# Kernel tuning notes

Measured on AMD Instinct MI355X. Metric: run time of the kernel, lower is better.

The kernel has to match this reference:

```python
import jax, jax.numpy as jnp
import numpy as np


def apply_rope(x):
    # x: [B, T, H, D]
    T, D = x.shape[1], x.shape[3]
    inv_freq = 1.0 / (10000.0 ** (jnp.arange(0, D, 2, dtype=jnp.float32) / D))  # [D/2]
    t = jnp.arange(T, dtype=jnp.float32)
    freqs = jnp.outer(t, inv_freq)  # [T, D/2]
    sin_f = jnp.sin(freqs)[None, :, None, :]
    cos_f = jnp.cos(freqs)[None, :, None, :]
    x1, x2 = jnp.split(x, 2, axis=-1)
    return jnp.concatenate([x1 * cos_f - x2 * sin_f, x1 * sin_f + x2 * cos_f], axis=-1)


def setup_inputs() -> dict:
    key = jax.random.key(0)
    ks = jax.random.split(key, 5)
    B, T, D = 8, 8192, 128
    s = 1.0 / np.sqrt(D)
    return {
        "x": jax.random.normal(ks[0], (B, T, D), dtype=jnp.float32),
        "Wq": jax.random.normal(ks[1], (D, D), dtype=jnp.float32) * s,
        "bq": jnp.zeros((D,), dtype=jnp.float32),
        "Wk": jax.random.normal(ks[2], (D, D), dtype=jnp.float32) * s,
        "bk": jnp.zeros((D,), dtype=jnp.float32),
        "Wv": jax.random.normal(ks[3], (D, D), dtype=jnp.float32) * s,
        "bv": jnp.zeros((D,), dtype=jnp.float32),
        "Wo": jax.random.normal(ks[4], (D, D), dtype=jnp.float32) * s,
        "bo": jnp.zeros((D,), dtype=jnp.float32),
    }


def reference(x, Wq, bq, Wk, bk, Wv, bv, Wo, bo):
    n_heads = 8
    B, T, d_model = x.shape
    head_dim = d_model // n_heads

    q = (x @ Wq + bq).reshape(B, T, n_heads, head_dim)
    k = (x @ Wk + bk).reshape(B, T, n_heads, head_dim)
    v = (x @ Wv + bv).reshape(B, T, n_heads, head_dim)

    q = jax.nn.elu(apply_rope(q)) + 1.0
    k = jax.nn.elu(apply_rope(k)) + 1.0

    # non-causal linear attention: context = sum_t k_t v_t^T per head
    context = jnp.einsum("bthd,bthe->bhde", k, v)            # [B,H,Dh,Dh]
    out = jnp.einsum("bthd,bhde->bthe", q, context)           # [B,T,H,Dh]
    k_sum = jnp.sum(k, axis=1)                                  # [B,H,Dh]
    z = 1.0 / (jnp.einsum("bthd,bhd->bth", q, k_sum) + 1e-6)  # [B,T,H]
    out = out * z[..., None]

    out = out.reshape(B, T, d_model)
    return out @ Wo + bo
```

## Files before the change

kernel.cpp:

```cpp
#include <hip/hip_runtime.h>
#include <hip/hip_bf16.h>


typedef __attribute__((ext_vector_type(8))) short short8;
typedef __attribute__((ext_vector_type(4))) float floatx4;

#define DEV __device__ __forceinline__
#define MFMA __builtin_amdgcn_mfma_f32_16x16x32_bf16

DEV unsigned short bfh(float f) {
  unsigned int x = __float_as_uint(f);
  x += 0x7fffu + ((x >> 16) & 1u);
  return (unsigned short)(x >> 16);
}
DEV float bfdec(unsigned short u) { return __uint_as_float(((unsigned int)u) << 16); }
DEV void splitf(float f, unsigned short& h, unsigned short& l) {
  h = bfh(f);
  l = bfh(f - bfdec(h));
}
DEV void split8(const float* p, short8& h8, short8& l8) {
  float4 a = *(const float4*)p;
  float4 b = *(const float4*)(p + 4);
  float v[8] = {a.x, a.y, a.z, a.w, b.x, b.y, b.z, b.w};
  union { short8 s; unsigned short u[8]; } H, L;
#pragma unroll
  for (int i = 0; i < 8; ++i) splitf(v[i], H.u[i], L.u[i]);
  h8 = H.s; l8 = L.s;
}

DEV void xpose_frag(floatx4 m0, floatx4 m1, int lane16, int quad,
                    short8& hi, short8& lo) {
  union { short8 s; unsigned short u[8]; } H, L;
#pragma unroll
  for (int j = 0; j < 8; ++j) {
    int srcLane = lane16 + (((quad & 1) * 2 + (j >> 2)) << 4);
    float vA = __shfl(m0[j & 3], srcLane, 64);
    float vB = __shfl(m1[j & 3], srcLane, 64);
    float v = (quad < 2) ? vA : vB;
    splitf(v, H.u[j], L.u[j]);
  }
  hi = H.s; lo = L.s;
}

DEV void async16(const void* g, void* l) {
  __builtin_amdgcn_global_load_lds(
      (const __attribute__((address_space(1))) unsigned int*)g,
      (__attribute__((address_space(3))) unsigned int*)l, 16, 0, 0);
}

__global__ void k_prep(const float* __restrict__ Wq, const float* __restrict__ Wk,
                       const float* __restrict__ Wv,
                       unsigned short* __restrict__ WTh, unsigned short* __restrict__ WTl,
                       float* __restrict__ ctxz) {
  int gid = blockIdx.x * 256 + threadIdx.x;
  if (gid < 6144) {
    int mat = gid >> 11, r = gid & 2047, n = r >> 4, k0 = (r & 15) * 8;
    const float* W = (mat == 0) ? Wq : (mat == 1) ? Wk : Wv;
    union { uint4 q; unsigned short u[8]; } oh, ol;
#pragma unroll
    for (int i = 0; i < 8; ++i) splitf(W[(size_t)(k0 + i) * 128 + n], oh.u[i], ol.u[i]);
    *(uint4*)&WTh[mat * 16384 + n * 128 + k0] = oh.q;
    *(uint4*)&WTl[mat * 16384 + n * 128 + k0] = ol.q;
  } else if (gid < 6144 + 17408) {
    ctxz[gid - 6144] = 0.0f;
  }
}

__global__ __launch_bounds__(512) void k_qkv(
    const float* __restrict__ x,
    const unsigned short* __restrict__ WTh, const unsigned short* __restrict__ WTl,
    const float* __restrict__ bq, const float* __restrict__ bk, const float* __restrict__ bv,
    float* __restrict__ ctx, float* __restrict__ ksum,
    unsigned short* __restrict__ qws) {
  __shared__ unsigned short xh[64 * 136], xl[64 * 136];
  __shared__ float rc[64][9], rs[64][9];
  const int tid = threadIdx.x;
  const int row0 = blockIdx.x * 64;
  const int b = row0 >> 13;
  const int t0 = row0 & 8191;

  {
    int r = tid >> 3, j = tid & 7;
    float invf = 1.0f / powf(10000.0f, (float)j * 0.125f);
    float s, c;
    sincosf((float)(t0 + r) * invf, &s, &c);
    rc[r][j] = c; rs[r][j] = s;
  }
  {
    int r = tid >> 3, cg = (tid & 7) * 16;
    const float* xp = x + (size_t)(row0 + r) * 128 + cg;
    short8 h0, l0, h1, l1;
    split8(xp, h0, l0);
    split8(xp + 8, h1, l1);
    *(short8*)&xh[r * 136 + cg] = h0;
    *(short8*)&xh[r * 136 + cg + 8] = h1;
    *(short8*)&xl[r * 136 + cg] = l0;
    *(short8*)&xl[r * 136 + cg + 8] = l1;
  }
  __syncthreads();

  const int l = tid & 63, w = tid >> 6;
  const int lane16 = l & 15, quad = l >> 4;

  floatx4 acc[3][4];
#pragma unroll
  for (int i = 0; i < 3; ++i)
#pragma unroll
    for (int j = 0; j < 4; ++j) acc[i][j] = (floatx4){0.f, 0.f, 0.f, 0.f};

  size_t wbase[3];
#pragma unroll
  for (int mat = 0; mat < 3; ++mat)
    wbase[mat] = (size_t)mat * 16384 + (size_t)(w * 16 + lane16) * 128 + quad * 8;

  short8 wh[2][3], wl[2][3];
#pragma unroll
  for (int mat = 0; mat < 3; ++mat) {
    wh[0][mat] = *(const short8*)(WTh + wbase[mat]);
    wl[0][mat] = *(const short8*)(WTl + wbase[mat]);
  }

#pragma unroll
  for (int ks = 0; ks < 4; ++ks) {
    const int cur = ks & 1, nxt = cur ^ 1;
    if (ks < 3) {
#pragma unroll
      for (int mat = 0; mat < 3; ++mat) {
        wh[nxt][mat] = *(const short8*)(WTh + wbase[mat] + (ks + 1) * 32);
        wl[nxt][mat] = *(const short8*)(WTl + wbase[mat] + (ks + 1) * 32);
      }
    }
    short8 afh[4], afl[4];
#pragma unroll
    for (int mt = 0; mt < 4; ++mt) {
      int off = (mt * 16 + lane16) * 136 + ks * 32 + quad * 8;
      afh[mt] = *(const short8*)&xh[off];
      afl[mt] = *(const short8*)&xl[off];
    }
#pragma unroll
    for (int mat = 0; mat < 3; ++mat) {
#pragma unroll
      for (int mt = 0; mt < 4; ++mt) {
        acc[mat][mt] = MFMA(afh[mt], wh[cur][mat], acc[mat][mt], 0, 0, 0);
        acc[mat][mt] = MFMA(afl[mt], wh[cur][mat], acc[mat][mt], 0, 0, 0);
        acc[mat][mt] = MFMA(afh[mt], wl[cur][mat], acc[mat][mt], 0, 0, 0);
      }
    }
  }

  {
    int col = w * 16 + lane16;
    float bias[3] = {bq[col], bk[col], bv[col]};
#pragma unroll
    for (int mat = 0; mat < 3; ++mat)
#pragma unroll
      for (int mt = 0; mt < 4; ++mt)
#pragma unroll
        for (int r = 0; r < 4; ++r) acc[mat][mt][r] += bias[mat];
  }

  {
    const int d = lane16, j = d & 7;
#pragma unroll
    for (int mt = 0; mt < 4; ++mt) {
      float cc[4], ss[4];
#pragma unroll
      for (int r = 0; r < 4; ++r) {
        int tl = mt * 16 + quad * 4 + r;
        cc[r] = rc[tl][j]; ss[r] = rs[tl][j];
      }
#pragma unroll
      for (int mat = 0; mat < 2; ++mat) {
#pragma unroll
        for (int r = 0; r < 4; ++r) {
          float v = acc[mat][mt][r];
          float p = __shfl_xor(v, 8);
          float nv = (d < 8) ? (v * cc[r] - p * ss[r]) : (p * ss[r] + v * cc[r]);
          acc[mat][mt][r] = (nv > 0.f) ? (nv + 1.f) : __expf(nv);
        }
      }
    }
  }

  {
    float s = 0.f;
#pragma unroll
    for (int mt = 0; mt < 4; ++mt)
#pragma unroll
      for (int r = 0; r < 4; ++r) s += acc[1][mt][r];
    s += __shfl_xor(s, 16);
    s += __shfl_xor(s, 32);
    if (l < 16) atomicAdd(&ksum[(b * 8 + w) * 16 + lane16], s);
  }

#pragma unroll
  for (int mt = 0; mt < 4; ++mt)
#pragma unroll
    for (int r = 0; r < 4; ++r)
      qws[(size_t)(row0 + mt * 16 + quad * 4 + r) * 128 + w * 16 + lane16] =
          bfh(acc[0][mt][r]);

  {
    floatx4 c = (floatx4){0.f, 0.f, 0.f, 0.f};
#pragma unroll
    for (int ks2 = 0; ks2 < 2; ++ks2) {
      short8 kh, kl, vh, vl;
      xpose_frag(acc[1][ks2 * 2], acc[1][ks2 * 2 + 1], lane16, quad, kh, kl);
      xpose_frag(acc[2][ks2 * 2], acc[2][ks2 * 2 + 1], lane16, quad, vh, vl);
      c = MFMA(kh, vh, c, 0, 0, 0);
      c = MFMA(kl, vh, c, 0, 0, 0);
      c = MFMA(kh, vl, c, 0, 0, 0);
    }
#pragma unroll
    for (int r = 0; r < 4; ++r)
      atomicAdd(&ctx[((size_t)(b * 8 + w) * 16 + quad * 4 + r) * 16 + lane16], c[r]);
  }
}

__global__ void k_mprep(const float* __restrict__ Wo, const float* __restrict__ ctx,
                        unsigned short* __restrict__ MTh, unsigned short* __restrict__ MTl) {
  int gid = blockIdx.x * 256 + threadIdx.x;
  int b = gid >> 11, r = gid & 2047, oc = r >> 4, qcg = r & 15;
  int h = qcg >> 1, d0 = (qcg & 1) * 8;
  const float* C = ctx + (size_t)(b * 8 + h) * 256;
  float m[8] = {0.f, 0.f, 0.f, 0.f, 0.f, 0.f, 0.f, 0.f};
#pragma unroll 4
  for (int e = 0; e < 16; ++e) {
    float wv = Wo[(size_t)(h * 16 + e) * 128 + oc];
#pragma unroll
    for (int i = 0; i < 8; ++i) m[i] += C[(d0 + i) * 16 + e] * wv;
  }
  union { uint4 q; unsigned short u[8]; } oh, ol;
#pragma unroll
  for (int i = 0; i < 8; ++i) splitf(m[i], oh.u[i], ol.u[i]);
  int grp = (((oc >> 4) * 4 + (qcg >> 2)) * 64) + (qcg & 3) * 16 + (oc & 15);
  *(uint4*)&MTh[(size_t)b * 16384 + grp * 8] = oh.q;
  *(uint4*)&MTl[(size_t)b * 16384 + grp * 8] = ol.q;
}

__global__ __launch_bounds__(256) void k_zout(
    const unsigned short* __restrict__ qws,
    const unsigned short* __restrict__ MTh, const unsigned short* __restrict__ MTl,
    const float* __restrict__ bo, const float* __restrict__ ksum,
    float* __restrict__ out) {
  __shared__ __align__(16) unsigned short mh[16384], ml[16384];
  __shared__ float ksumS[128], boS[128];
  const int tid = threadIdx.x;
  const int row0 = blockIdx.x * 128;
  const int b = row0 >> 13;
  const int l = tid & 63, w = tid >> 6;
  const int lane16 = l & 15, quad = l >> 4;

  {
    const char* gh = (const char*)(MTh + (size_t)b * 16384);
    const char* gl = (const char*)(MTl + (size_t)b * 16384);
#pragma unroll
    for (int i = 0; i < 8; ++i) {
      int off = (i * 4 + w) * 1024 + l * 16;
      async16(gh + off, (char*)mh + off);
      async16(gl + off, (char*)ml + off);
    }
  }
  if (tid < 128) ksumS[tid] = ksum[b * 128 + tid];
  else boS[tid - 128] = bo[tid - 128];
  __syncthreads();

  short8 ah[2][4], al[2][4];
#pragma unroll
  for (int mt2 = 0; mt2 < 2; ++mt2) {
    int trow = row0 + w * 32 + mt2 * 16 + lane16;
#pragma unroll
    for (int ks = 0; ks < 4; ++ks) {
      union { short8 s8; unsigned short u[8]; } qq;
      qq.s8 = *(const short8*)&qws[(size_t)trow * 128 + ks * 32 + quad * 8];
      int kb = ks * 32 + quad * 8;
      float s = 0.f;
#pragma unroll
      for (int j = 0; j < 8; ++j) s += bfdec(qq.u[j]) * ksumS[kb + j];
      s += __shfl_xor(s, 16);
      float z = 1.0f / (s + 1e-6f);
      union { short8 s8; unsigned short u[8]; } H, L;
#pragma unroll
      for (int j = 0; j < 8; ++j) splitf(bfdec(qq.u[j]) * z, H.u[j], L.u[j]);
      ah[mt2][ks] = H.s8;
      al[mt2][ks] = L.s8;
    }
  }

  floatx4 oacc[2][8];
#pragma unroll
  for (int i = 0; i < 2; ++i)
#pragma unroll
    for (int j = 0; j < 8; ++j) oacc[i][j] = (floatx4){0.f, 0.f, 0.f, 0.f};

#pragma unroll
  for (int nt = 0; nt < 8; ++nt) {
#pragma unroll
    for (int ks = 0; ks < 4; ++ks) {
      int moff = ((nt * 4 + ks) * 64 + l) * 8;
      short8 wbh = *(const short8*)&mh[moff];
      short8 wbl = *(const short8*)&ml[moff];
#pragma unroll
      for (int mt2 = 0; mt2 < 2; ++mt2) {
        oacc[mt2][nt] = MFMA(ah[mt2][ks], wbh, oacc[mt2][nt], 0, 0, 0);
        oacc[mt2][nt] = MFMA(al[mt2][ks], wbh, oacc[mt2][nt], 0, 0, 0);
        oacc[mt2][nt] = MFMA(ah[mt2][ks], wbl, oacc[mt2][nt], 0, 0, 0);
      }
    }
  }

#pragma unroll
  for (int nt = 0; nt < 8; ++nt) {
    int oc = nt * 16 + lane16;
    float bb = boS[oc];
#pragma unroll
    for (int mt2 = 0; mt2 < 2; ++mt2)
#pragma unroll
      for (int r = 0; r < 4; ++r) {
        int t = row0 + w * 32 + mt2 * 16 + quad * 4 + r;
        out[(size_t)t * 128 + oc] = oacc[mt2][nt][r] + bb;
      }
  }
}

extern "C" void kernel_launch(void* const* d_in, const int* in_sizes, int n_in,
                              void* d_out, int out_size, void* d_ws, size_t ws_size,
                              hipStream_t stream) {
  const float* x  = (const float*)d_in[0];
  const float* Wq = (const float*)d_in[1];
  const float* bq = (const float*)d_in[2];
  const float* Wk = (const float*)d_in[3];
  const float* bk = (const float*)d_in[4];
  const float* Wv = (const float*)d_in[5];
  const float* bv = (const float*)d_in[6];
  const float* Wo = (const float*)d_in[7];
  const float* bo = (const float*)d_in[8];
  float* out = (float*)d_out;

  unsigned short* qws = (unsigned short*)d_ws;
  unsigned short* WTh = qws + 8388608;
  unsigned short* WTl = WTh + 49152;
  float* ctx  = (float*)(WTl + 49152);
  float* ksum = ctx + 16384;
  unsigned short* MTh = (unsigned short*)(ksum + 1024);
  unsigned short* MTl = MTh + 131072;

  k_prep<<<92, 256, 0, stream>>>(Wq, Wk, Wv, WTh, WTl, ctx);
  k_qkv<<<1024, 512, 0, stream>>>(x, WTh, WTl, bq, bk, bv, ctx, ksum, qws);
  k_mprep<<<64, 256, 0, stream>>>(Wo, ctx, MTh, MTl);
  k_zout<<<512, 256, 0, stream>>>(qws, MTh, MTl, bo, ksum, out);
}
```

Measured before the change: 159.4 us.

## Drop x low-part split in QKV, precompute RoPE table, widen zout blocks

The QKV projection now rounds x to a single bf16 part instead of a hi/lo split. This removes one of the three MFMAs per tile, the xl shared buffer and the split arithmetic, at the cost of accuracy on the activation side. RoPE sin/cos values are precomputed once into a workspace table in k_prep rather than evaluated per block with powf/sincosf. k_zout moves to 512 threads with one 16-row tile per wave, lowering register use per thread in exchange for more waves per block.

```diff
diff --git a/kernel.cpp b/kernel.cpp
--- a/kernel.cpp
+++ b/kernel.cpp
@@ -17,15 +17,6 @@
 DEV void splitf(float f, unsigned short& h, unsigned short& l) {
   h = bfh(f);
   l = bfh(f - bfdec(h));
-}
-DEV void split8(const float* p, short8& h8, short8& l8) {
-  float4 a = *(const float4*)p;
-  float4 b = *(const float4*)(p + 4);
-  float v[8] = {a.x, a.y, a.z, a.w, b.x, b.y, b.z, b.w};
-  union { short8 s; unsigned short u[8]; } H, L;
-#pragma unroll
-  for (int i = 0; i < 8; ++i) splitf(v[i], H.u[i], L.u[i]);
-  h8 = H.s; l8 = L.s;
 }
 
 DEV void xpose_frag(floatx4 m0, floatx4 m1, int lane16, int quad,
@@ -51,7 +42,7 @@
 __global__ void k_prep(const float* __restrict__ Wq, const float* __restrict__ Wk,
                        const float* __restrict__ Wv,
                        unsigned short* __restrict__ WTh, unsigned short* __restrict__ WTl,
-                       float* __restrict__ ctxz) {
+                       float* __restrict__ ctxz, float2* __restrict__ ropeT) {
   int gid = blockIdx.x * 256 + threadIdx.x;
   if (gid < 6144) {
     int mat = gid >> 11, r = gid & 2047, n = r >> 4, k0 = (r & 15) * 8;
@@ -63,16 +54,23 @@
     *(uint4*)&WTl[mat * 16384 + n * 128 + k0] = ol.q;
   } else if (gid < 6144 + 17408) {
     ctxz[gid - 6144] = 0.0f;
+  } else if (gid < 6144 + 17408 + 65536) {
+    int r = gid - 23552;
+    int t = r >> 3, j = r & 7;
+    float invf = 1.0f / powf(10000.0f, (float)j * 0.125f);
+    float s, c;
+    sincosf((float)t * invf, &s, &c);
+    ropeT[r] = make_float2(c, s);
   }
 }
 
 __global__ __launch_bounds__(512) void k_qkv(
-    const float* __restrict__ x,
+    const float* __restrict__ x, const float2* __restrict__ ropeT,
     const unsigned short* __restrict__ WTh, const unsigned short* __restrict__ WTl,
     const float* __restrict__ bq, const float* __restrict__ bk, const float* __restrict__ bv,
     float* __restrict__ ctx, float* __restrict__ ksum,
     unsigned short* __restrict__ qws) {
-  __shared__ unsigned short xh[64 * 136], xl[64 * 136];
+  __shared__ unsigned short xh[64 * 136];
   __shared__ float rc[64][9], rs[64][9];
   const int tid = threadIdx.x;
   const int row0 = blockIdx.x * 64;
@@ -81,21 +79,23 @@
 
   {
     int r = tid >> 3, j = tid & 7;
-    float invf = 1.0f / powf(10000.0f, (float)j * 0.125f);
-    float s, c;
-    sincosf((float)(t0 + r) * invf, &s, &c);
-    rc[r][j] = c; rs[r][j] = s;
+    float2 cs = ropeT[(t0 + r) * 8 + j];
+    rc[r][j] = cs.x; rs[r][j] = cs.y;
   }
   {
     int r = tid >> 3, cg = (tid & 7) * 16;
     const float* xp = x + (size_t)(row0 + r) * 128 + cg;
-    short8 h0, l0, h1, l1;
-    split8(xp, h0, l0);
-    split8(xp + 8, h1, l1);
-    *(short8*)&xh[r * 136 + cg] = h0;
-    *(short8*)&xh[r * 136 + cg + 8] = h1;
-    *(short8*)&xl[r * 136 + cg] = l0;
-    *(short8*)&xl[r * 136 + cg + 8] = l1;
+    float4 a = *(const float4*)xp;
+    float4 b4 = *(const float4*)(xp + 4);
+    float4 c4 = *(const float4*)(xp + 8);
+    float4 d4 = *(const float4*)(xp + 12);
+    float v[16] = {a.x, a.y, a.z, a.w, b4.x, b4.y, b4.z, b4.w,
+                   c4.x, c4.y, c4.z, c4.w, d4.x, d4.y, d4.z, d4.w};
+    union { short8 s; unsigned short u[8]; } h0, h1;
+#pragma unroll
+    for (int i = 0; i < 8; ++i) { h0.u[i] = bfh(v[i]); h1.u[i] = bfh(v[8 + i]); }
+    *(short8*)&xh[r * 136 + cg] = h0.s;
+    *(short8*)&xh[r * 136 + cg + 8] = h1.s;
   }
   __syncthreads();
 
@@ -130,19 +130,15 @@
         wl[nxt][mat] = *(const short8*)(WTl + wbase[mat] + (ks + 1) * 32);
       }
     }
-    short8 afh[4], afl[4];
-#pragma unroll
-    for (int mt = 0; mt < 4; ++mt) {
-      int off = (mt * 16 + lane16) * 136 + ks * 32 + quad * 8;
-      afh[mt] = *(const short8*)&xh[off];
-      afl[mt] = *(const short8*)&xl[off];
-    }
+    short8 afh[4];
+#pragma unroll
+    for (int mt = 0; mt < 4; ++mt)
+      afh[mt] = *(const short8*)&xh[(mt * 16 + lane16) * 136 + ks * 32 + quad * 8];
 #pragma unroll
     for (int mat = 0; mat < 3; ++mat) {
 #pragma unroll
       for (int mt = 0; mt < 4; ++mt) {
         acc[mat][mt] = MFMA(afh[mt], wh[cur][mat], acc[mat][mt], 0, 0, 0);
-        acc[mat][mt] = MFMA(afl[mt], wh[cur][mat], acc[mat][mt], 0, 0, 0);
         acc[mat][mt] = MFMA(afh[mt], wl[cur][mat], acc[mat][mt], 0, 0, 0);
       }
     }
@@ -238,7 +234,7 @@
   *(uint4*)&MTl[(size_t)b * 16384 + grp * 8] = ol.q;
 }
 
-__global__ __launch_bounds__(256) void k_zout(
+__global__ __launch_bounds__(512) void k_zout(
     const unsigned short* __restrict__ qws,
     const unsigned short* __restrict__ MTh, const unsigned short* __restrict__ MTl,
     const float* __restrict__ bo, const float* __restrict__ ksum,
@@ -255,43 +251,38 @@
     const char* gh = (const char*)(MTh + (size_t)b * 16384);
     const char* gl = (const char*)(MTl + (size_t)b * 16384);
 #pragma unroll
-    for (int i = 0; i < 8; ++i) {
-      int off = (i * 4 + w) * 1024 + l * 16;
+    for (int i = 0; i < 4; ++i) {
+      int off = (i * 8 + w) * 1024 + l * 16;
       async16(gh + off, (char*)mh + off);
       async16(gl + off, (char*)ml + off);
     }
   }
   if (tid < 128) ksumS[tid] = ksum[b * 128 + tid];
-  else boS[tid - 128] = bo[tid - 128];
+  else if (tid < 256) boS[tid - 128] = bo[tid - 128];
   __syncthreads();
 
-  short8 ah[2][4], al[2][4];
-#pragma unroll
-  for (int mt2 = 0; mt2 < 2; ++mt2) {
-    int trow = row0 + w * 32 + mt2 * 16 + lane16;
-#pragma unroll
-    for (int ks = 0; ks < 4; ++ks) {
-      union { short8 s8; unsigned short u[8]; } qq;
-      qq.s8 = *(const short8*)&qws[(size_t)trow * 128 + ks * 32 + quad * 8];
-      int kb = ks * 32 + quad * 8;
-      float s = 0.f;
-#pragma unroll
-      for (int j = 0; j < 8; ++j) s += bfdec(qq.u[j]) * ksumS[kb + j];
-      s += __shfl_xor(s, 16);
-      float z = 1.0f / (s + 1e-6f);
-      union { short8 s8; unsigned short u[8]; } H, L;
-#pragma unroll
-      for (int j = 0; j < 8; ++j) splitf(bfdec(qq.u[j]) * z, H.u[j], L.u[j]);
-      ah[mt2][ks] = H.s8;
-      al[mt2][ks] = L.s8;
-    }
-  }
-
-  floatx4 oacc[2][8];
-#pragma unroll
-  for (int i = 0; i < 2; ++i)
-#pragma unroll
-    for (int j = 0; j < 8; ++j) oacc[i][j] = (floatx4){0.f, 0.f, 0.f, 0.f};
+  const int trow = row0 + w * 16 + lane16;
+  short8 ah[4], al[4];
+#pragma unroll
+  for (int ks = 0; ks < 4; ++ks) {
+    union { short8 s8; unsigned short u[8]; } qq;
+    qq.s8 = *(const short8*)&qws[(size_t)trow * 128 + ks * 32 + quad * 8];
+    int kb = ks * 32 + quad * 8;
+    float s = 0.f;
+#pragma unroll
+    for (int j = 0; j < 8; ++j) s += bfdec(qq.u[j]) * ksumS[kb + j];
+    s += __shfl_xor(s, 16);
+    float z = 1.0f / (s + 1e-6f);
+    union { short8 s8; unsigned short u[8]; } H, L;
+#pragma unroll
+    for (int j = 0; j < 8; ++j) splitf(bfdec(qq.u[j]) * z, H.u[j], L.u[j]);
+    ah[ks] = H.s8;
+    al[ks] = L.s8;
+  }
+
+  floatx4 oacc[8];
+#pragma unroll
+  for (int j = 0; j < 8; ++j) oacc[j] = (floatx4){0.f, 0.f, 0.f, 0.f};
 
 #pragma unroll
   for (int nt = 0; nt < 8; ++nt) {
@@ -300,12 +291,9 @@
       int moff = ((nt * 4 + ks) * 64 + l) * 8;
       short8 wbh = *(const short8*)&mh[moff];
       short8 wbl = *(const short8*)&ml[moff];
-#pragma unroll
-      for (int mt2 = 0; mt2 < 2; ++mt2) {
-        oacc[mt2][nt] = MFMA(ah[mt2][ks], wbh, oacc[mt2][nt], 0, 0, 0);
-        oacc[mt2][nt] = MFMA(al[mt2][ks], wbh, oacc[mt2][nt], 0, 0, 0);
-        oacc[mt2][nt] = MFMA(ah[mt2][ks], wbl, oacc[mt2][nt], 0, 0, 0);
-      }
+      oacc[nt] = MFMA(ah[ks], wbh, oacc[nt], 0, 0, 0);
+      oacc[nt] = MFMA(al[ks], wbh, oacc[nt], 0, 0, 0);
+      oacc[nt] = MFMA(ah[ks], wbl, oacc[nt], 0, 0, 0);
     }
   }
 
@@ -314,12 +302,10 @@
     int oc = nt * 16 + lane16;
     float bb = boS[oc];
 #pragma unroll
-    for (int mt2 = 0; mt2 < 2; ++mt2)
-#pragma unroll
-      for (int r = 0; r < 4; ++r) {
-        int t = row0 + w * 32 + mt2 * 16 + quad * 4 + r;
-        out[(size_t)t * 128 + oc] = oacc[mt2][nt][r] + bb;
-      }
+    for (int r = 0; r < 4; ++r) {
+      int t = row0 + w * 16 + quad * 4 + r;
+      out[(size_t)t * 128 + oc] = oacc[nt][r] + bb;
+    }
   }
 }
 
@@ -344,9 +330,10 @@
   float* ksum = ctx + 16384;
   unsigned short* MTh = (unsigned short*)(ksum + 1024);
   unsigned short* MTl = MTh + 131072;
-
-  k_prep<<<92, 256, 0, stream>>>(Wq, Wk, Wv, WTh, WTl, ctx);
-  k_qkv<<<1024, 512, 0, stream>>>(x, WTh, WTl, bq, bk, bv, ctx, ksum, qws);
+  float2* ropeT = (float2*)(MTl + 131072);
+
+  k_prep<<<348, 256, 0, stream>>>(Wq, Wk, Wv, WTh, WTl, ctx, ropeT);
+  k_qkv<<<1024, 512, 0, stream>>>(x, ropeT, WTh, WTl, bq, bk, bv, ctx, ksum, qws);
   k_mprep<<<64, 256, 0, stream>>>(Wo, ctx, MTh, MTl);
-  k_zout<<<512, 256, 0, stream>>>(qws, MTh, MTl, bo, ksum, out);
-}
+  k_zout<<<512, 512, 0, stream>>>(qws, MTh, MTl, bo, ksum, out);
+}
```

Measured after the change: 159.8 us. About the same (+0.3%).
